# Kernel tuning notes

Measured on AMD Instinct MI355X. Metric: run time of the kernel, lower is better.

The kernel has to match this reference:

```python
import jax, jax.numpy as jnp
import numpy as np

MOE_TOP_K = 2
MOE_GATE_NORM_STD = 1.0  # moe_gate_norm_std


def setup_inputs() -> dict:
    key = jax.random.key(0)
    k1, k2, k3, k4 = jax.random.split(key, 4)
    T, D, E = 16384, 2048, 8
    return {
        "x": jax.random.normal(k1, (T, D), dtype=jnp.float32),
        "wg_weight": jax.random.normal(k2, (E, D), dtype=jnp.float32) * 0.02,
        "gate_map_weight": jax.random.normal(k3, (E, E), dtype=jnp.float32) * 0.1,
        "gate_residual": jax.random.normal(k4, (T, E), dtype=jnp.float32),
    }


def reference(x, wg_weight, gate_map_weight, gate_residual):
    # Router GEMM in fp32 (module force-casts wg and input to float32)
    logits = jnp.einsum("td,ed->te", x.astype(jnp.float32), wg_weight)  # [T, E]
    # gate_residual path: gate_map Linear(E, E, bias=False)
    logits = logits + jnp.einsum("te,fe->tf", gate_residual, gate_map_weight)

    num_experts = wg_weight.shape[0]
    # gating(): moe_use_mixtral_gating=False, moe_use_logits_norm=True
    # torch.std is unbiased (ddof=1)
    logits_std = jnp.std(logits, axis=1, keepdims=True, ddof=1)
    probs = jax.nn.softmax(logits / (logits_std / MOE_GATE_NORM_STD), axis=1)
    gates, indices = jax.lax.top_k(probs, MOE_TOP_K)  # [T, K]
    # zero out routing to the last expert, then renormalize
    gates = jnp.where(indices == num_experts - 1, jnp.zeros_like(gates), gates)
    gates = gates / jnp.sum(gates, axis=1, keepdims=True)
    # Dense equivalent of the per-expert nonzero-gather dict: (indices, gates)
    # fully determines expert_info[e] = (tokens where indices==e, matching gates).
    return gates, indices, logits
```

## Files before the change

kernel.cpp:

```cpp
#include <hip/hip_runtime.h>
#include <hip/hip_bf16.h>
#include <stdint.h>


#define WAVES_PER_BLOCK 4
#define TOKENS_PER_WAVE 8
#define TOKENS_PER_BLOCK (WAVES_PER_BLOCK * TOKENS_PER_WAVE)

__device__ __forceinline__ unsigned long long shfl_xor_u64(unsigned long long v, int m) {
    int lo = __shfl_xor((int)(uint32_t)v, m, 64);
    int hi = __shfl_xor((int)(uint32_t)(v >> 32), m, 64);
    return ((unsigned long long)(uint32_t)hi << 32) | (unsigned long long)(uint32_t)lo;
}

__global__ __launch_bounds__(256, 2)
void router_kernel(const float* __restrict__ x,
                   const float* __restrict__ wg,
                   const float* __restrict__ gm,
                   const float* __restrict__ gr,
                   float* __restrict__ out,
                   int T, int D)
{
    const int wave = threadIdx.x >> 6;
    const int lane = threadIdx.x & 63;
    const int t0   = blockIdx.x * TOKENS_PER_BLOCK + wave * TOKENS_PER_WAVE;

    __shared__ float sc_all[WAVES_PER_BLOCK][32 * 65];
    float* sc = sc_all[wave];

    float acc[8][8];
    #pragma unroll
    for (int tt = 0; tt < 8; ++tt)
        #pragma unroll
        for (int e = 0; e < 8; ++e) acc[tt][e] = 0.f;

    const float* xw  = x  + (size_t)t0 * D + lane * 4;
    const float* wgl = wg + lane * 4;

    #pragma unroll
    for (int j = 0; j < 8; ++j) {
        float4 xf[8];
        #pragma unroll
        for (int tt = 0; tt < 8; ++tt)
            xf[tt] = *(const float4*)(xw + (size_t)tt * D + j * 256);
        #pragma unroll
        for (int e = 0; e < 8; ++e) {
            const float4 wf = *(const float4*)(wgl + (size_t)e * D + j * 256);
            #pragma unroll
            for (int tt = 0; tt < 8; ++tt) {
                acc[tt][e] += xf[tt].x * wf.x;
                acc[tt][e] += xf[tt].y * wf.y;
                acc[tt][e] += xf[tt].z * wf.z;
                acc[tt][e] += xf[tt].w * wf.w;
            }
        }
    }

    float logit = 0.f;
    #pragma unroll
    for (int ph = 0; ph < 2; ++ph) {
        __syncthreads();
        #pragma unroll
        for (int v = 0; v < 32; ++v) {
            const int vv = ph * 32 + v;
            sc[v * 65 + lane] = acc[vv >> 3][vv & 7];
        }
        __syncthreads();
        const int vrow = lane & 31;
        const int half = lane >> 5;
        float r0 = 0.f, r1 = 0.f, r2 = 0.f, r3 = 0.f;
        const float* row = sc + vrow * 65 + half * 32;
        #pragma unroll
        for (int j = 0; j < 32; j += 4) {
            r0 += row[j];
            r1 += row[j + 1];
            r2 += row[j + 2];
            r3 += row[j + 3];
        }
        float h = (r0 + r1) + (r2 + r3);
        h += __shfl_xor(h, 32, 64);
        if ((lane >> 5) == ph) logit = h;
    }

    const int tt = lane >> 3;
    const int f  = lane & 7;
    const int t  = t0 + tt;

    const float4 ga = *(const float4*)(gr + (size_t)t * 8);
    const float4 gb = *(const float4*)(gr + (size_t)t * 8 + 4);
    const float4 ma = *(const float4*)(gm + f * 8);
    const float4 mb = *(const float4*)(gm + f * 8 + 4);
    logit += ga.x * ma.x + ga.y * ma.y + ga.z * ma.z + ga.w * ma.w
           + gb.x * mb.x + gb.y * mb.y + gb.z * mb.z + gb.w * mb.w;

    out[(size_t)4 * T + (size_t)t0 * 8 + lane] = logit;

    float s = logit;
    s += __shfl_xor(s, 1, 64);
    s += __shfl_xor(s, 2, 64);
    s += __shfl_xor(s, 4, 64);
    const float mean = s * 0.125f;
    float d2 = (logit - mean) * (logit - mean);
    d2 += __shfl_xor(d2, 1, 64);
    d2 += __shfl_xor(d2, 2, 64);
    d2 += __shfl_xor(d2, 4, 64);
    const float stdv = sqrtf(d2 / 7.0f);

    uint32_t ob = __float_as_uint(logit);
    ob = (ob & 0x80000000u) ? ~ob : (ob | 0x80000000u);
    unsigned long long k1 = ((unsigned long long)ob << 8) | (unsigned long long)(7 - f);
    unsigned long long k2 = 0ull;
    #pragma unroll
    for (int m = 1; m <= 4; m <<= 1) {
        const unsigned long long o1 = shfl_xor_u64(k1, m);
        const unsigned long long o2 = shfl_xor_u64(k2, m);
        const unsigned long long hi = k1 > o1 ? k1 : o1;
        const unsigned long long lo = k1 > o1 ? o1 : k1;
        const unsigned long long so = k2 > o2 ? k2 : o2;
        k1 = hi;
        k2 = lo > so ? lo : so;
    }
    const int i1 = 7 - (int)(k1 & 0xFFull);
    const int i2 = 7 - (int)(k2 & 0xFFull);
    uint32_t b1 = (uint32_t)(k1 >> 8), b2 = (uint32_t)(k2 >> 8);
    b1 = (b1 & 0x80000000u) ? (b1 ^ 0x80000000u) : ~b1;
    b2 = (b2 & 0x80000000u) ? (b2 ^ 0x80000000u) : ~b2;
    const float l1 = __uint_as_float(b1);
    const float l2 = __uint_as_float(b2);

    float g0, g1;
    if (i1 == 7)      { g0 = 0.f; g1 = 1.f; }
    else if (i2 == 7) { g0 = 1.f; g1 = 0.f; }
    else {
        const float p = 1.0f / (1.0f + __expf(-(l1 - l2) / stdv));
        g0 = p; g1 = 1.0f - p;
    }

    if (f == 0) out[(size_t)2 * t]             = g0;
    if (f == 1) out[(size_t)2 * t + 1]         = g1;
    if (f == 2) out[(size_t)2 * T + 2 * t]     = (float)i1;
    if (f == 3) out[(size_t)2 * T + 2 * t + 1] = (float)i2;
}

extern "C" void kernel_launch(void* const* d_in, const int* in_sizes, int n_in,
                              void* d_out, int out_size, void* d_ws, size_t ws_size,
                              hipStream_t stream) {
    const float* x  = (const float*)d_in[0];
    const float* wg = (const float*)d_in[1];
    const float* gm = (const float*)d_in[2];
    const float* gr = (const float*)d_in[3];
    const int E = 8;
    const int D = in_sizes[1] / E;
    const int T = in_sizes[0] / D;
    const int blocks = T / TOKENS_PER_BLOCK;
    router_kernel<<<blocks, 256, 0, stream>>>(x, wg, gm, gr, (float*)d_out, T, D);
}
```

Before: 206.9 us.

## Stage gate weights in LDS, double-buffer x loads, shuffle-based transpose reduction

Each block copies the full 8x2048 gate weight matrix into 64KB of shared memory, then reads weights from LDS instead of global/L2. The x loads are software-pipelined with two register buffers so the next chunk's loads overlap the current chunk's FMAs. The LDS transpose reduction is replaced by a butterfly shuffle reduce-scatter, so each lane ends up holding one logit. D is hardcoded to 2048. The cost is 64KB of LDS per block, which limits occupancy, and a redundant weight copy in every block.

```diff
diff --git a/kernel.cpp b/kernel.cpp
--- a/kernel.cpp
+++ b/kernel.cpp
@@ -6,6 +6,8 @@
 #define WAVES_PER_BLOCK 4
 #define TOKENS_PER_WAVE 8
 #define TOKENS_PER_BLOCK (WAVES_PER_BLOCK * TOKENS_PER_WAVE)
+#define DCONST 2048
+#define NCHUNK 8
 
 __device__ __forceinline__ unsigned long long shfl_xor_u64(unsigned long long v, int m) {
     int lo = __shfl_xor((int)(uint32_t)v, m, 64);
@@ -19,68 +21,73 @@
                    const float* __restrict__ gm,
                    const float* __restrict__ gr,
                    float* __restrict__ out,
-                   int T, int D)
+                   int T)
 {
     const int wave = threadIdx.x >> 6;
     const int lane = threadIdx.x & 63;
     const int t0   = blockIdx.x * TOKENS_PER_BLOCK + wave * TOKENS_PER_WAVE;
 
-    __shared__ float sc_all[WAVES_PER_BLOCK][32 * 65];
-    float* sc = sc_all[wave];
+    __shared__ float swg[8 * DCONST];
+    {
+        const float4* src = (const float4*)wg;
+        float4*       dst = (float4*)swg;
+        #pragma unroll
+        for (int i = 0; i < 16; ++i)
+            dst[threadIdx.x + i * 256] = src[threadIdx.x + i * 256];
+    }
+    __syncthreads();
 
-    float acc[8][8];
+    float acc[64];
     #pragma unroll
-    for (int tt = 0; tt < 8; ++tt)
-        #pragma unroll
-        for (int e = 0; e < 8; ++e) acc[tt][e] = 0.f;
+    for (int v = 0; v < 64; ++v) acc[v] = 0.f;
 
-    const float* xw  = x  + (size_t)t0 * D + lane * 4;
-    const float* wgl = wg + lane * 4;
+    const float* xw = x + (size_t)t0 * DCONST + (lane << 2);
+    const float* wl = swg + (lane << 2);
+
+    float4 xa[8], xb[8];
+
+    #define LOADX(buf, j)                                                     \
+        { _Pragma("unroll")                                                   \
+          for (int tt = 0; tt < 8; ++tt)                                      \
+              buf[tt] = *(const float4*)(xw + tt * DCONST + (j) * 256); }
+
+    #define COMPUTE(j, buf)                                                   \
+        { _Pragma("unroll")                                                   \
+          for (int e = 0; e < 8; ++e) {                                       \
+              const float4 wf = *(const float4*)(wl + e * DCONST + (j) * 256);\
+              _Pragma("unroll")                                               \
+              for (int tt = 0; tt < 8; ++tt) {                                \
+                  acc[tt * 8 + e] += buf[tt].x * wf.x;                        \
+                  acc[tt * 8 + e] += buf[tt].y * wf.y;                        \
+                  acc[tt * 8 + e] += buf[tt].z * wf.z;                        \
+                  acc[tt * 8 + e] += buf[tt].w * wf.w;                        \
+              }                                                               \
+          } }
+
+    LOADX(xa, 0);
+    #pragma unroll 1
+    for (int j = 0; j < NCHUNK - 2; j += 2) {
+        LOADX(xb, j + 1);
+        COMPUTE(j, xa);
+        LOADX(xa, j + 2);
+        COMPUTE(j + 1, xb);
+    }
+    LOADX(xb, NCHUNK - 1);
+    COMPUTE(NCHUNK - 2, xa);
+    COMPUTE(NCHUNK - 1, xb);
 
     #pragma unroll
-    for (int j = 0; j < 8; ++j) {
-        float4 xf[8];
+    for (int m = 1; m < 64; m <<= 1) {
+        const bool up = (lane & m) != 0;
         #pragma unroll
-        for (int tt = 0; tt < 8; ++tt)
-            xf[tt] = *(const float4*)(xw + (size_t)tt * D + j * 256);
-        #pragma unroll
-        for (int e = 0; e < 8; ++e) {
-            const float4 wf = *(const float4*)(wgl + (size_t)e * D + j * 256);
-            #pragma unroll
-            for (int tt = 0; tt < 8; ++tt) {
-                acc[tt][e] += xf[tt].x * wf.x;
-                acc[tt][e] += xf[tt].y * wf.y;
-                acc[tt][e] += xf[tt].z * wf.z;
-                acc[tt][e] += xf[tt].w * wf.w;
-            }
+        for (int v = 0; v < 64; v += 2 * m) {
+            const float keep = up ? acc[v + m] : acc[v];
+            const float send = up ? acc[v] : acc[v + m];
+            const float got  = __shfl_xor(send, m, 64);
+            acc[v] = keep + got;
         }
     }
-
-    float logit = 0.f;
-    #pragma unroll
-    for (int ph = 0; ph < 2; ++ph) {
-        __syncthreads();
-        #pragma unroll
-        for (int v = 0; v < 32; ++v) {
-            const int vv = ph * 32 + v;
-            sc[v * 65 + lane] = acc[vv >> 3][vv & 7];
-        }
-        __syncthreads();
-        const int vrow = lane & 31;
-        const int half = lane >> 5;
-        float r0 = 0.f, r1 = 0.f, r2 = 0.f, r3 = 0.f;
-        const float* row = sc + vrow * 65 + half * 32;
-        #pragma unroll
-        for (int j = 0; j < 32; j += 4) {
-            r0 += row[j];
-            r1 += row[j + 1];
-            r2 += row[j + 2];
-            r3 += row[j + 3];
-        }
-        float h = (r0 + r1) + (r2 + r3);
-        h += __shfl_xor(h, 32, 64);
-        if ((lane >> 5) == ph) logit = h;
-    }
+    float logit = acc[0];
 
     const int tt = lane >> 3;
     const int f  = lane & 7;
@@ -149,9 +156,7 @@
     const float* wg = (const float*)d_in[1];
     const float* gm = (const float*)d_in[2];
     const float* gr = (const float*)d_in[3];
-    const int E = 8;
-    const int D = in_sizes[1] / E;
-    const int T = in_sizes[0] / D;
+    const int T = in_sizes[0] / DCONST;
     const int blocks = T / TOKENS_PER_BLOCK;
-    router_kernel<<<blocks, 256, 0, stream>>>(x, wg, gm, gr, (float*)d_out, T, D);
+    router_kernel<<<blocks, 256, 0, stream>>>(x, wg, gm, gr, (float*)d_out, T);
 }
```

Result: faster. 195.4 us (-5.6%).
